# Kernel tuning notes

Hardware: AMD Instinct MI355X
Metric: run time of the kernel (lower is better)

The kernel has to match this reference:

```python
import jax, jax.numpy as jnp
import numpy as np

WS = 8            # window_size
SHIFT = WS // 2   # cyclic shift for 'SW' type
HEAD_DIM = 32

def _rel_index(ws):
    # pairwise relative coordinate indices within a window, offset to [0, 2ws-2]
    cord = np.array([[i, j] for i in range(ws) for j in range(ws)])
    rel = cord[:, None, :] - cord[None, :, :] + ws - 1
    return rel[:, :, 0], rel[:, :, 1]

def _shift_mask(h_w, w_w, p):
    # boolean attention mask for shifted windows; True = masked (-inf)
    s = p - SHIFT
    m = np.zeros((h_w, w_w, p, p, p, p), dtype=bool)
    m[-1, :, :s, :, s:, :] = True
    m[-1, :, s:, :, :s, :] = True
    m[:, -1, :, :s, :, s:] = True
    m[:, -1, :, s:, :, :s] = True
    return m.reshape(h_w * w_w, p * p, p * p)

def setup_inputs() -> dict:
    key = jax.random.key(0)
    ks = jax.random.split(key, 6)
    b, H, W, c = 4, 256, 256, 256
    nh = c // HEAD_DIM
    return {
        "x": jax.random.normal(ks[0], (b, H, W, c), jnp.float32),
        "W_qkv": jax.random.normal(ks[1], (c, 3 * c), jnp.float32) * 0.02,
        "b_qkv": jnp.zeros((3 * c,), jnp.float32),
        "rel_pos": jax.random.normal(ks[2], (nh, 2 * WS - 1, 2 * WS - 1), jnp.float32) * 0.02,
        "W_out": jax.random.normal(ks[3], (c, c), jnp.float32) * 0.02,
        "b_out": jnp.zeros((c,), jnp.float32),
    }

def reference(x, W_qkv, b_qkv, rel_pos, W_out, b_out):
    b, H, W, c = x.shape
    nh = c // HEAD_DIM
    scale = HEAD_DIM ** -0.5
    # cyclic shift (type == 'SW')
    x = jnp.roll(x, (-SHIFT, -SHIFT), axis=(1, 2))
    hw, ww = H // WS, W // WS
    nw, p2 = hw * ww, WS * WS
    # partition into windows: [b, nw, p2, c]
    xw = x.reshape(b, hw, WS, ww, WS, c).transpose(0, 1, 3, 2, 4, 5).reshape(b, nw, p2, c)
    # QKV projection; layout of out dim is (3, n_heads, head_dim)
    qkv = (xw @ W_qkv + b_qkv).reshape(b, nw, p2, 3, nh, HEAD_DIM)
    q, k, v = qkv[..., 0, :, :], qkv[..., 1, :, :], qkv[..., 2, :, :]
    # attention scores per head/window: [h, b, nw, p2, p2]
    sim = jnp.einsum('bwphc,bwqhc->hbwpq', q, k) * scale
    ri, rj = _rel_index(WS)
    sim = sim + rel_pos[:, ri, rj][:, None, None]            # relative position bias
    mask = jnp.asarray(_shift_mask(hw, ww, WS))              # [nw, p2, p2]
    sim = jnp.where(mask[None, None], -jnp.inf, sim)
    probs = jax.nn.softmax(sim, axis=-1)
    out = jnp.einsum('hbwpq,bwqhc->bwphc', probs, v).reshape(b, nw, p2, nh * HEAD_DIM)
    out = out @ W_out + b_out
    # un-window: [b, H, W, c_out]
    out = out.reshape(b, hw, ww, WS, WS, -1).transpose(0, 1, 3, 2, 4, 5).reshape(b, H, W, -1)
    return jnp.roll(out, (SHIFT, SHIFT), axis=(1, 2))
```

## Files before the change

kernel.cpp:

```cpp
#include <hip/hip_runtime.h>
#include <hip/hip_bf16.h>

typedef __attribute__((ext_vector_type(4))) float f32x4;
typedef __attribute__((ext_vector_type(2))) unsigned int u32x2;
typedef __attribute__((ext_vector_type(8))) short s16x8;
typedef __attribute__((ext_vector_type(8))) __bf16 bf16v8;
typedef __attribute__((ext_vector_type(8))) _Float16 f16v8;
typedef __attribute__((ext_vector_type(4))) _Float16 f16x4;

#define LDS_XS 0
#define LDS_QS 32768
#define LDS_KS 65536
#define LDS_VT 98304
#define LDS_TOT 131072

__device__ __forceinline__ f32x4 mfma16(s16x8 a, s16x8 b, f32x4 c) {
  return __builtin_amdgcn_mfma_f32_16x16x32_bf16(
      __builtin_bit_cast(bf16v8, a), __builtin_bit_cast(bf16v8, b), c, 0, 0, 0);
}
__device__ __forceinline__ f32x4 mfma16h(s16x8 a, s16x8 b, f32x4 c) {
  return __builtin_amdgcn_mfma_f32_16x16x32_f16(
      __builtin_bit_cast(f16v8, a), __builtin_bit_cast(f16v8, b), c, 0, 0, 0);
}
__device__ __forceinline__ f32x4 mfmah16(f16x4 a, f16x4 b, f32x4 c) {
  return __builtin_amdgcn_mfma_f32_16x16x16f16(a, b, c, 0, 0, 0);
}

__device__ __forceinline__ unsigned int cvt2(float a, float b) {
  __hip_bfloat162 r = __float22bfloat162_rn(make_float2(a, b));
  unsigned int u;
  __builtin_memcpy(&u, &r, 4);
  return u;
}
__device__ __forceinline__ unsigned int cvt2h(float a, float b) {
  auto r = __builtin_amdgcn_cvt_pkrtz(a, b);
  unsigned int u;
  __builtin_memcpy(&u, &r, 4);
  return u;
}
__device__ __forceinline__ f16x4 pack4h(float a, float b, float c, float d) {
  u32x2 u;
  u.x = cvt2h(a, b);
  u.y = cvt2h(c, d);
  f16x4 r;
  __builtin_memcpy(&r, &u, 8);
  return r;
}

__device__ __forceinline__ short f2bf(float f) {
  unsigned u = __float_as_uint(f);
  u += 0x7fffu + ((u >> 16) & 1u);
  return (short)(u >> 16);
}

__device__ __forceinline__ int swz512(int row, int colByte) {
  return row * 512 + (colByte ^ ((row & 7) << 4));
}
__device__ __forceinline__ int swz128(int row, int colByte) {
  return row * 128 + (colByte ^ ((row & 7) << 4));
}

__global__ void prep_w(const float* __restrict__ Wqkv, const float* __restrict__ Wout,
                       const float* __restrict__ relp,
                       short* __restrict__ wqkvT, short* __restrict__ wH,
                       float* __restrict__ relt) {
  int t = blockIdx.x * 256 + threadIdx.x;
  if (t < 768 * 256) {
    int n = t >> 8, k = t & 255;
    wqkvT[t] = f2bf(Wqkv[k * 768 + n]);
  } else if (t < 768 * 256 + 256 * 256) {
    int t2 = t - 768 * 256;
    int n = t2 >> 8, k = t2 & 255;
    _Float16 h = (_Float16)Wout[k * 256 + n];
    unsigned short us;
    __builtin_memcpy(&us, &h, 2);
    wH[t2] = (short)us;
  } else {
    int u = t - 768 * 256 - 256 * 256;
    int r = u & 3, l = (u >> 2) & 63, strip = (u >> 8) & 3;
    int qt = (u >> 10) & 3, h = (u >> 12) & 7, var = (u >> 15) & 3;
    int p = strip * 16 + (l & 15);
    int q = qt * 16 + ((l >> 4) << 2) + r;
    int pi = p >> 3, pj = p & 7, qi = q >> 3, qj = q & 7;
    bool mrow = (var >> 1) & 1, mcol = var & 1;
    bool mk = (mrow && ((pi < 4) != (qi < 4))) || (mcol && ((pj < 4) != (qj < 4)));
    relt[u] = mk ? -1e30f : relp[h * 225 + (pi - qi + 7) * 15 + (pj - qj + 7)];
  }
}

__global__ __launch_bounds__(512, 2) void swin_mfma(
    const float* __restrict__ x, const float* __restrict__ bqkv,
    const float* __restrict__ bout,
    const short* __restrict__ wqkvT, const short* __restrict__ wH,
    const float* __restrict__ relt, float* __restrict__ out)
{
  __shared__ __align__(16) char lds[LDS_TOT];

  const int tx = threadIdx.x;
  const int w  = tx >> 6;
  const int l  = tx & 63;
  const int g  = l >> 4;
  const int li = l & 15;

  const int b   = blockIdx.x >> 10;
  const int wdw = blockIdx.x & 1023;
  const int wh  = wdw >> 5, wwi = wdw & 31;
  const int rvar = ((wh == 31) ? 2 : 0) | ((wwi == 31) ? 1 : 0);
  const int phalf = w & 1, p0 = phalf * 32;

  for (int i = 0; i < 8; ++i) {
    int idx = tx + i * 512;
    int p = idx >> 6, c4 = idx & 63;
    int pi = p >> 3, pj = p & 7;
    int sr = (wh * 8 + pi + 4) & 255;
    int sc = (wwi * 8 + pj + 4) & 255;
    f32x4 v = *(const f32x4*)(x + ((((size_t)b * 256 + sr) * 256 + sc) * 256 + c4 * 4));
    u32x2 uu;
    uu.x = cvt2(v[0], v[1]);
    uu.y = cvt2(v[2], v[3]);
    *(u32x2*)(lds + LDS_XS + swz512(p, c4 * 8)) = uu;
  }

  int ocol[6];
  #pragma unroll
  for (int j = 0; j < 4; ++j) ocol[j] = (w * 4 + j) * 16 + li;
  #pragma unroll
  for (int j = 4; j < 6; ++j) ocol[j] = 512 + (w * 2 + (j - 4)) * 16 + li;
  s16x8 bcur[6];
  #pragma unroll
  for (int j = 0; j < 6; ++j)
    bcur[j] = *(const s16x8*)(wqkvT + (size_t)ocol[j] * 256 + g * 8);

  __syncthreads();

  {
    f32x4 acc[6][4];
    #pragma unroll
    for (int j = 0; j < 6; ++j)
      #pragma unroll
      for (int rb = 0; rb < 4; ++rb)
        acc[j][rb] = (f32x4){0.f, 0.f, 0.f, 0.f};

    s16x8 a[2][4];
    #pragma unroll
    for (int rb = 0; rb < 4; ++rb)
      a[0][rb] = *(const s16x8*)(lds + LDS_XS + swz512(rb * 16 + li, g * 16));

    #pragma unroll
    for (int kk = 0; kk < 8; ++kk) {
      const int cur = kk & 1;
      s16x8 bnext[6];
      if (kk < 7) {
        #pragma unroll
        for (int rb = 0; rb < 4; ++rb)
          a[cur ^ 1][rb] = *(const s16x8*)(lds + LDS_XS
                                           + swz512(rb * 16 + li, (kk + 1) * 64 + g * 16));
        #pragma unroll
        for (int j = 0; j < 6; ++j)
          bnext[j] = *(const s16x8*)(wqkvT + (size_t)ocol[j] * 256 + (kk + 1) * 32 + g * 8);
      }
      #pragma unroll
      for (int j = 0; j < 4; ++j)
        #pragma unroll
        for (int rb = 0; rb < 4; ++rb)
          acc[j][rb] = mfma16(bcur[j], a[cur][rb], acc[j][rb]);
      #pragma unroll
      for (int j = 4; j < 6; ++j)
        #pragma unroll
        for (int rb = 0; rb < 4; ++rb)
          acc[j][rb] = mfma16(a[cur][rb], bcur[j], acc[j][rb]);
      if (kk < 7) {
        #pragma unroll
        for (int j = 0; j < 6; ++j) bcur[j] = bnext[j];
      }
    }

    #pragma unroll
    for (int j = 0; j < 4; ++j) {
      const int cb = w * 4 + j;
      if (cb < 16) {
        f32x4 bq = *(const f32x4*)(bqkv + cb * 16 + g * 4);
        #pragma unroll
        for (int rb = 0; rb < 4; ++rb) {
          const float SC = 0.17677669529663687f;
          u32x2 uu;
          uu.x = cvt2((acc[j][rb][0] + bq[0]) * SC, (acc[j][rb][1] + bq[1]) * SC);
          uu.y = cvt2((acc[j][rb][2] + bq[2]) * SC, (acc[j][rb][3] + bq[3]) * SC);
          *(u32x2*)(lds + LDS_QS + swz512(rb * 16 + li, cb * 32 + g * 8)) = uu;
        }
      } else {
        f32x4 bk = *(const f32x4*)(bqkv + cb * 16 + g * 4);
        #pragma unroll
        for (int rb = 0; rb < 4; ++rb) {
          u32x2 uu;
          uu.x = cvt2(acc[j][rb][0] + bk[0], acc[j][rb][1] + bk[1]);
          uu.y = cvt2(acc[j][rb][2] + bk[2], acc[j][rb][3] + bk[3]);
          *(u32x2*)(lds + LDS_KS + swz512(rb * 16 + li, (cb - 16) * 32 + g * 8)) = uu;
        }
      }
    }
    #pragma unroll
    for (int j = 4; j < 6; ++j) {
      const int d = (w * 2 + (j - 4)) * 16 + li;
      const float bv = bqkv[512 + d];
      #pragma unroll
      for (int rb = 0; rb < 4; ++rb) {
        u32x2 uu;
        uu.x = cvt2h(acc[j][rb][0] + bv, acc[j][rb][1] + bv);
        uu.y = cvt2h(acc[j][rb][2] + bv, acc[j][rb][3] + bv);
        *(u32x2*)(lds + LDS_VT + swz128(d, rb * 32 + g * 8)) = uu;
      }
    }
  }

  f32x4 rc2[2][2][4];
  #pragma unroll
  for (int u = 0; u < 2; ++u) {
    const int h = (w >> 1) + u * 4;
    #pragma unroll
    for (int pt = 0; pt < 2; ++pt)
      #pragma unroll
      for (int qt = 0; qt < 4; ++qt)
        rc2[u][pt][qt] = *(const f32x4*)(relt
            + ((((rvar * 8 + h) * 4 + qt) * 4 + (phalf * 2 + pt)) * 64 + l) * 4);
  }

  __syncthreads();

  {
    s16x8 qf2[2][2], kf2[2][4];
    f16x4 vf2[2][2][4];
    #pragma unroll
    for (int u = 0; u < 2; ++u) {
      const int h = (w >> 1) + u * 4;
      #pragma unroll
      for (int pt = 0; pt < 2; ++pt)
        qf2[u][pt] = *(const s16x8*)(lds + LDS_QS + swz512(p0 + pt * 16 + li, h * 64 + g * 16));
      #pragma unroll
      for (int qt = 0; qt < 4; ++qt)
        kf2[u][qt] = *(const s16x8*)(lds + LDS_KS + swz512(qt * 16 + li, h * 64 + g * 16));
      #pragma unroll
      for (int dt = 0; dt < 2; ++dt)
        #pragma unroll
        for (int qt = 0; qt < 4; ++qt)
          vf2[u][dt][qt] = *(const f16x4*)(lds + LDS_VT
                                           + swz128(h * 32 + dt * 16 + li, qt * 32 + g * 8));
    }

    #pragma unroll
    for (int u = 0; u < 2; ++u) {
      const int h = (w >> 1) + u * 4;

      f32x4 simT[2][4];
      #pragma unroll
      for (int pt = 0; pt < 2; ++pt)
        #pragma unroll
        for (int qt = 0; qt < 4; ++qt)
          simT[pt][qt] = mfma16(kf2[u][qt], qf2[u][pt], rc2[u][pt][qt]);

      float rinv[2];
      f16x4 pa[2][4];
      #pragma unroll
      for (int pt = 0; pt < 2; ++pt) {
        float s = 0.f;
        #pragma unroll
        for (int qt = 0; qt < 4; ++qt) {
          float e0 = __expf(simT[pt][qt][0]);
          float e1 = __expf(simT[pt][qt][1]);
          float e2 = __expf(simT[pt][qt][2]);
          float e3 = __expf(simT[pt][qt][3]);
          s += (e0 + e1) + (e2 + e3);
          pa[pt][qt] = pack4h(e0, e1, e2, e3);
        }
        s += __shfl_xor(s, 16);
        s += __shfl_xor(s, 32);
        rinv[pt] = 1.0f / s;
      }

      f32x4 at[2][2];
      #pragma unroll
      for (int pt = 0; pt < 2; ++pt)
        #pragma unroll
        for (int dt = 0; dt < 2; ++dt)
          at[pt][dt] = (f32x4){0.f, 0.f, 0.f, 0.f};
      #pragma unroll
      for (int qt = 0; qt < 4; ++qt)
        #pragma unroll
        for (int pt = 0; pt < 2; ++pt)
          #pragma unroll
          for (int dt = 0; dt < 2; ++dt)
            at[pt][dt] = mfmah16(vf2[u][dt][qt], pa[pt][qt], at[pt][dt]);

      #pragma unroll
      for (int pt = 0; pt < 2; ++pt)
        #pragma unroll
        for (int dt = 0; dt < 2; ++dt) {
          const f32x4 a4 = at[pt][dt];
          u32x2 hh;
          hh.x = cvt2h(a4[0] * rinv[pt], a4[1] * rinv[pt]);
          hh.y = cvt2h(a4[2] * rinv[pt], a4[3] * rinv[pt]);
          *(u32x2*)(lds + LDS_XS + swz512(p0 + pt * 16 + li, h * 64 + dt * 32 + g * 8)) = hh;
        }
    }
  }

  s16x8 bc[2];
  #pragma unroll
  for (int c = 0; c < 2; ++c)
    bc[c] = *(const s16x8*)(wH + (size_t)((w * 2 + c) * 16 + li) * 256 + g * 8);

  __syncthreads();

  {
    f32x4 acc2[2][4];
    #pragma unroll
    for (int c = 0; c < 2; ++c)
      #pragma unroll
      for (int rb = 0; rb < 4; ++rb)
        acc2[c][rb] = (f32x4){0.f, 0.f, 0.f, 0.f};

    s16x8 a[2][4];
    #pragma unroll
    for (int rb = 0; rb < 4; ++rb)
      a[0][rb] = *(const s16x8*)(lds + LDS_XS + swz512(rb * 16 + li, g * 16));

    #pragma unroll
    for (int kk = 0; kk < 8; ++kk) {
      const int cur = kk & 1;
      s16x8 bn[2];
      if (kk < 7) {
        #pragma unroll
        for (int rb = 0; rb < 4; ++rb)
          a[cur ^ 1][rb] = *(const s16x8*)(lds + LDS_XS
                                           + swz512(rb * 16 + li, (kk + 1) * 64 + g * 16));
        #pragma unroll
        for (int c = 0; c < 2; ++c)
          bn[c] = *(const s16x8*)(wH + (size_t)((w * 2 + c) * 16 + li) * 256
                                  + (kk + 1) * 32 + g * 8);
      }
      #pragma unroll
      for (int c = 0; c < 2; ++c)
        #pragma unroll
        for (int rb = 0; rb < 4; ++rb)
          acc2[c][rb] = mfma16h(a[cur][rb], bc[c], acc2[c][rb]);
      if (kk < 7) {
        #pragma unroll
        for (int c = 0; c < 2; ++c) bc[c] = bn[c];
      }
    }

    #pragma unroll
    for (int c = 0; c < 2; ++c) {
      const int n = (w * 2 + c) * 16 + li;
      const float bo = bout[n];
      #pragma unroll
      for (int rb = 0; rb < 4; ++rb)
        #pragma unroll
        for (int r = 0; r < 4; ++r) {
          int m = rb * 16 + g * 4 + r;
          int pi = m >> 3, pj = m & 7;
          int dr = (wh * 8 + pi + 4) & 255;
          int dc = (wwi * 8 + pj + 4) & 255;
          out[(((size_t)b * 256 + dr) * 256 + dc) * 256 + n] = acc2[c][rb][r] + bo;
        }
    }
  }
}

extern "C" void kernel_launch(void* const* d_in, const int* in_sizes, int n_in,
                              void* d_out, int out_size, void* d_ws, size_t ws_size,
                              hipStream_t stream) {
  (void)in_sizes; (void)n_in; (void)out_size; (void)ws_size;
  const float* x    = (const float*)d_in[0];
  const float* Wqkv = (const float*)d_in[1];
  const float* bqkv = (const float*)d_in[2];
  const float* relp = (const float*)d_in[3];
  const float* Wout = (const float*)d_in[4];
  const float* bout = (const float*)d_in[5];
  float* out = (float*)d_out;

  short* wqkvT = (short*)d_ws;
  short* wH    = wqkvT + 768 * 256;
  float* relt  = (float*)(wH + 256 * 256);

  hipLaunchKernelGGL(prep_w, dim3(1536), dim3(256), 0, stream,
                     Wqkv, Wout, relp, wqkvT, wH, relt);
  hipLaunchKernelGGL(swin_mfma, dim3(4096), dim3(512), 0, stream,
                     x, bqkv, bout, wqkvT, wH, relt, out);
}
```

Baseline: 397.7 us.

## Make swin kernel persistent over 16 windows with async prefetch of next window

The kernel now launches 256 blocks that each loop over 16 consecutive windows instead of one block per window. During the output projection of each window, the next window's fp32 input is fetched straight into LDS with global_load_lds, then converted to bf16 after a barrier. The aim is to hide global input latency behind MFMA work and to avoid per-block launch and prologue costs. The trade-off is that 256 blocks at 2 blocks/CU may underfill the GPU, and the loop adds extra barriers and a serial convert step per window.

```diff
diff --git a/kernel.cpp b/kernel.cpp
--- a/kernel.cpp
+++ b/kernel.cpp
@@ -88,6 +88,38 @@
   }
 }
 
+__device__ __forceinline__ void stage_x_async(const float* __restrict__ x, int win,
+                                              int w, int l, char* lds) {
+  const int b = win >> 10, wdw = win & 1023;
+  const int wh = wdw >> 5, wwi = wdw & 31;
+  #pragma unroll
+  for (int i = 0; i < 8; ++i) {
+    const int chunk = (w * 8 + i) * 64 + l;
+    const int p = chunk >> 6, c4 = chunk & 63;
+    const int pi = p >> 3, pj = p & 7;
+    const int sr = (wh * 8 + pi + 4) & 255;
+    const int sc = (wwi * 8 + pj + 4) & 255;
+    const float* gsrc = x + ((((size_t)b * 256 + sr) * 256 + sc) * 256 + c4 * 4);
+    __builtin_amdgcn_global_load_lds(
+        (const __attribute__((address_space(1))) void*)gsrc,
+        (__attribute__((address_space(3))) void*)(lds + LDS_QS + (w * 8 + i) * 1024),
+        16, 0, 0);
+  }
+}
+
+__device__ __forceinline__ void convert_x(int tx, char* lds) {
+  #pragma unroll
+  for (int i = 0; i < 8; ++i) {
+    const int chunk = tx + i * 512;
+    f32x4 v = *(const f32x4*)(lds + LDS_QS + chunk * 16);
+    const int p = chunk >> 6, c4 = chunk & 63;
+    u32x2 uu;
+    uu.x = cvt2(v[0], v[1]);
+    uu.y = cvt2(v[2], v[3]);
+    *(u32x2*)(lds + LDS_XS + swz512(p, c4 * 8)) = uu;
+  }
+}
+
 __global__ __launch_bounds__(512, 2) void swin_mfma(
     const float* __restrict__ x, const float* __restrict__ bqkv,
     const float* __restrict__ bout,
@@ -101,268 +133,271 @@
   const int l  = tx & 63;
   const int g  = l >> 4;
   const int li = l & 15;
-
-  const int b   = blockIdx.x >> 10;
-  const int wdw = blockIdx.x & 1023;
-  const int wh  = wdw >> 5, wwi = wdw & 31;
-  const int rvar = ((wh == 31) ? 2 : 0) | ((wwi == 31) ? 1 : 0);
   const int phalf = w & 1, p0 = phalf * 32;
-
-  for (int i = 0; i < 8; ++i) {
-    int idx = tx + i * 512;
-    int p = idx >> 6, c4 = idx & 63;
-    int pi = p >> 3, pj = p & 7;
-    int sr = (wh * 8 + pi + 4) & 255;
-    int sc = (wwi * 8 + pj + 4) & 255;
-    f32x4 v = *(const f32x4*)(x + ((((size_t)b * 256 + sr) * 256 + sc) * 256 + c4 * 4));
-    u32x2 uu;
-    uu.x = cvt2(v[0], v[1]);
-    uu.y = cvt2(v[2], v[3]);
-    *(u32x2*)(lds + LDS_XS + swz512(p, c4 * 8)) = uu;
-  }
 
   int ocol[6];
   #pragma unroll
   for (int j = 0; j < 4; ++j) ocol[j] = (w * 4 + j) * 16 + li;
   #pragma unroll
   for (int j = 4; j < 6; ++j) ocol[j] = 512 + (w * 2 + (j - 4)) * 16 + li;
-  s16x8 bcur[6];
-  #pragma unroll
-  for (int j = 0; j < 6; ++j)
-    bcur[j] = *(const s16x8*)(wqkvT + (size_t)ocol[j] * 256 + g * 8);
-
+
+  stage_x_async(x, blockIdx.x * 16, w, l, lds);
   __syncthreads();
-
-  {
-    f32x4 acc[6][4];
-    #pragma unroll
-    for (int j = 0; j < 6; ++j)
+  convert_x(tx, lds);
+  __syncthreads();
+
+  #pragma unroll 1
+  for (int wi = 0; wi < 16; ++wi) {
+    const int win = blockIdx.x * 16 + wi;
+    const int b   = win >> 10;
+    const int wdw = win & 1023;
+    const int wh  = wdw >> 5, wwi = wdw & 31;
+    const int rvar = ((wh == 31) ? 2 : 0) | ((wwi == 31) ? 1 : 0);
+
+    {
+      f32x4 acc[6][4];
+      #pragma unroll
+      for (int j = 0; j < 6; ++j)
+        #pragma unroll
+        for (int rb = 0; rb < 4; ++rb)
+          acc[j][rb] = (f32x4){0.f, 0.f, 0.f, 0.f};
+
+      s16x8 bcur[6];
+      #pragma unroll
+      for (int j = 0; j < 6; ++j)
+        bcur[j] = *(const s16x8*)(wqkvT + (size_t)ocol[j] * 256 + g * 8);
+
+      s16x8 a[2][4];
       #pragma unroll
       for (int rb = 0; rb < 4; ++rb)
-        acc[j][rb] = (f32x4){0.f, 0.f, 0.f, 0.f};
-
-    s16x8 a[2][4];
-    #pragma unroll
-    for (int rb = 0; rb < 4; ++rb)
-      a[0][rb] = *(const s16x8*)(lds + LDS_XS + swz512(rb * 16 + li, g * 16));
-
-    #pragma unroll
-    for (int kk = 0; kk < 8; ++kk) {
-      const int cur = kk & 1;
-      s16x8 bnext[6];
-      if (kk < 7) {
-        #pragma unroll
-        for (int rb = 0; rb < 4; ++rb)
-          a[cur ^ 1][rb] = *(const s16x8*)(lds + LDS_XS
-                                           + swz512(rb * 16 + li, (kk + 1) * 64 + g * 16));
-        #pragma unroll
-        for (int j = 0; j < 6; ++j)
-          bnext[j] = *(const s16x8*)(wqkvT + (size_t)ocol[j] * 256 + (kk + 1) * 32 + g * 8);
-      }
-      #pragma unroll
-      for (int j = 0; j < 4; ++j)
-        #pragma unroll
-        for (int rb = 0; rb < 4; ++rb)
-          acc[j][rb] = mfma16(bcur[j], a[cur][rb], acc[j][rb]);
-      #pragma unroll
-      for (int j = 4; j < 6; ++j)
-        #pragma unroll
-        for (int rb = 0; rb < 4; ++rb)
-          acc[j][rb] = mfma16(a[cur][rb], bcur[j], acc[j][rb]);
-      if (kk < 7) {
-        #pragma unroll
-        for (int j = 0; j < 6; ++j) bcur[j] = bnext[j];
-      }
-    }
-
-    #pragma unroll
-    for (int j = 0; j < 4; ++j) {
-      const int cb = w * 4 + j;
-      if (cb < 16) {
-        f32x4 bq = *(const f32x4*)(bqkv + cb * 16 + g * 4);
-        #pragma unroll
-        for (int rb = 0; rb < 4; ++rb) {
-          const float SC = 0.17677669529663687f;
-          u32x2 uu;
-          uu.x = cvt2((acc[j][rb][0] + bq[0]) * SC, (acc[j][rb][1] + bq[1]) * SC);
-          uu.y = cvt2((acc[j][rb][2] + bq[2]) * SC, (acc[j][rb][3] + bq[3]) * SC);
-          *(u32x2*)(lds + LDS_QS + swz512(rb * 16 + li, cb * 32 + g * 8)) = uu;
-        }
-      } else {
-        f32x4 bk = *(const f32x4*)(bqkv + cb * 16 + g * 4);
+        a[0][rb] = *(const s16x8*)(lds + LDS_XS + swz512(rb * 16 + li, g * 16));
+
+      #pragma unroll
+      for (int kk = 0; kk < 8; ++kk) {
+        const int cur = kk & 1;
+        s16x8 bnext[6];
+        if (kk < 7) {
+          #pragma unroll
+          for (int rb = 0; rb < 4; ++rb)
+            a[cur ^ 1][rb] = *(const s16x8*)(lds + LDS_XS
+                                             + swz512(rb * 16 + li, (kk + 1) * 64 + g * 16));
+          #pragma unroll
+          for (int j = 0; j < 6; ++j)
+            bnext[j] = *(const s16x8*)(wqkvT + (size_t)ocol[j] * 256 + (kk + 1) * 32 + g * 8);
+        }
+        #pragma unroll
+        for (int j = 0; j < 4; ++j)
+          #pragma unroll
+          for (int rb = 0; rb < 4; ++rb)
+            acc[j][rb] = mfma16(bcur[j], a[cur][rb], acc[j][rb]);
+        #pragma unroll
+        for (int j = 4; j < 6; ++j)
+          #pragma unroll
+          for (int rb = 0; rb < 4; ++rb)
+            acc[j][rb] = mfma16(a[cur][rb], bcur[j], acc[j][rb]);
+        if (kk < 7) {
+          #pragma unroll
+          for (int j = 0; j < 6; ++j) bcur[j] = bnext[j];
+        }
+      }
+
+      #pragma unroll
+      for (int j = 0; j < 4; ++j) {
+        const int cb = w * 4 + j;
+        if (cb < 16) {
+          f32x4 bq = *(const f32x4*)(bqkv + cb * 16 + g * 4);
+          #pragma unroll
+          for (int rb = 0; rb < 4; ++rb) {
+            const float SC = 0.17677669529663687f;
+            u32x2 uu;
+            uu.x = cvt2((acc[j][rb][0] + bq[0]) * SC, (acc[j][rb][1] + bq[1]) * SC);
+            uu.y = cvt2((acc[j][rb][2] + bq[2]) * SC, (acc[j][rb][3] + bq[3]) * SC);
+            *(u32x2*)(lds + LDS_QS + swz512(rb * 16 + li, cb * 32 + g * 8)) = uu;
+          }
+        } else {
+          f32x4 bk = *(const f32x4*)(bqkv + cb * 16 + g * 4);
+          #pragma unroll
+          for (int rb = 0; rb < 4; ++rb) {
+            u32x2 uu;
+            uu.x = cvt2(acc[j][rb][0] + bk[0], acc[j][rb][1] + bk[1]);
+            uu.y = cvt2(acc[j][rb][2] + bk[2], acc[j][rb][3] + bk[3]);
+            *(u32x2*)(lds + LDS_KS + swz512(rb * 16 + li, (cb - 16) * 32 + g * 8)) = uu;
+          }
+        }
+      }
+      #pragma unroll
+      for (int j = 4; j < 6; ++j) {
+        const int d = (w * 2 + (j - 4)) * 16 + li;
+        const float bv = bqkv[512 + d];
         #pragma unroll
         for (int rb = 0; rb < 4; ++rb) {
           u32x2 uu;
-          uu.x = cvt2(acc[j][rb][0] + bk[0], acc[j][rb][1] + bk[1]);
-          uu.y = cvt2(acc[j][rb][2] + bk[2], acc[j][rb][3] + bk[3]);
-          *(u32x2*)(lds + LDS_KS + swz512(rb * 16 + li, (cb - 16) * 32 + g * 8)) = uu;
+          uu.x = cvt2h(acc[j][rb][0] + bv, acc[j][rb][1] + bv);
+          uu.y = cvt2h(acc[j][rb][2] + bv, acc[j][rb][3] + bv);
+          *(u32x2*)(lds + LDS_VT + swz128(d, rb * 32 + g * 8)) = uu;
         }
       }
     }
-    #pragma unroll
-    for (int j = 4; j < 6; ++j) {
-      const int d = (w * 2 + (j - 4)) * 16 + li;
-      const float bv = bqkv[512 + d];
-      #pragma unroll
-      for (int rb = 0; rb < 4; ++rb) {
-        u32x2 uu;
-        uu.x = cvt2h(acc[j][rb][0] + bv, acc[j][rb][1] + bv);
-        uu.y = cvt2h(acc[j][rb][2] + bv, acc[j][rb][3] + bv);
-        *(u32x2*)(lds + LDS_VT + swz128(d, rb * 32 + g * 8)) = uu;
-      }
-    }
-  }
-
-  f32x4 rc2[2][2][4];
-  #pragma unroll
-  for (int u = 0; u < 2; ++u) {
-    const int h = (w >> 1) + u * 4;
-    #pragma unroll
-    for (int pt = 0; pt < 2; ++pt)
-      #pragma unroll
-      for (int qt = 0; qt < 4; ++qt)
-        rc2[u][pt][qt] = *(const f32x4*)(relt
-            + ((((rvar * 8 + h) * 4 + qt) * 4 + (phalf * 2 + pt)) * 64 + l) * 4);
-  }
-
-  __syncthreads();
-
-  {
-    s16x8 qf2[2][2], kf2[2][4];
-    f16x4 vf2[2][2][4];
+
+    f32x4 rc2[2][2][4];
     #pragma unroll
     for (int u = 0; u < 2; ++u) {
       const int h = (w >> 1) + u * 4;
       #pragma unroll
       for (int pt = 0; pt < 2; ++pt)
-        qf2[u][pt] = *(const s16x8*)(lds + LDS_QS + swz512(p0 + pt * 16 + li, h * 64 + g * 16));
-      #pragma unroll
-      for (int qt = 0; qt < 4; ++qt)
-        kf2[u][qt] = *(const s16x8*)(lds + LDS_KS + swz512(qt * 16 + li, h * 64 + g * 16));
-      #pragma unroll
-      for (int dt = 0; dt < 2; ++dt)
         #pragma unroll
         for (int qt = 0; qt < 4; ++qt)
-          vf2[u][dt][qt] = *(const f16x4*)(lds + LDS_VT
-                                           + swz128(h * 32 + dt * 16 + li, qt * 32 + g * 8));
+          rc2[u][pt][qt] = *(const f32x4*)(relt
+              + ((((rvar * 8 + h) * 4 + qt) * 4 + (phalf * 2 + pt)) * 64 + l) * 4);
     }
 
-    #pragma unroll
-    for (int u = 0; u < 2; ++u) {
-      const int h = (w >> 1) + u * 4;
-
-      f32x4 simT[2][4];
-      #pragma unroll
-      for (int pt = 0; pt < 2; ++pt)
+    __syncthreads();
+
+    {
+      s16x8 qf2[2][2], kf2[2][4];
+      f16x4 vf2[2][2][4];
+      #pragma unroll
+      for (int u = 0; u < 2; ++u) {
+        const int h = (w >> 1) + u * 4;
+        #pragma unroll
+        for (int pt = 0; pt < 2; ++pt)
+          qf2[u][pt] = *(const s16x8*)(lds + LDS_QS + swz512(p0 + pt * 16 + li, h * 64 + g * 16));
         #pragma unroll
         for (int qt = 0; qt < 4; ++qt)
-          simT[pt][qt] = mfma16(kf2[u][qt], qf2[u][pt], rc2[u][pt][qt]);
-
-      float rinv[2];
-      f16x4 pa[2][4];
-      #pragma unroll
-      for (int pt = 0; pt < 2; ++pt) {
-        float s = 0.f;
-        #pragma unroll
-        for (int qt = 0; qt < 4; ++qt) {
-          float e0 = __expf(simT[pt][qt][0]);
-          float e1 = __expf(simT[pt][qt][1]);
-          float e2 = __expf(simT[pt][qt][2]);
-          float e3 = __expf(simT[pt][qt][3]);
-          s += (e0 + e1) + (e2 + e3);
-          pa[pt][qt] = pack4h(e0, e1, e2, e3);
-        }
-        s += __shfl_xor(s, 16);
-        s += __shfl_xor(s, 32);
-        rinv[pt] = 1.0f / s;
-      }
-
-      f32x4 at[2][2];
-      #pragma unroll
-      for (int pt = 0; pt < 2; ++pt)
+          kf2[u][qt] = *(const s16x8*)(lds + LDS_KS + swz512(qt * 16 + li, h * 64 + g * 16));
         #pragma unroll
         for (int dt = 0; dt < 2; ++dt)
-          at[pt][dt] = (f32x4){0.f, 0.f, 0.f, 0.f};
-      #pragma unroll
-      for (int qt = 0; qt < 4; ++qt)
+          #pragma unroll
+          for (int qt = 0; qt < 4; ++qt)
+            vf2[u][dt][qt] = *(const f16x4*)(lds + LDS_VT
+                                             + swz128(h * 32 + dt * 16 + li, qt * 32 + g * 8));
+      }
+
+      #pragma unroll
+      for (int u = 0; u < 2; ++u) {
+        const int h = (w >> 1) + u * 4;
+
+        f32x4 simT[2][4];
         #pragma unroll
         for (int pt = 0; pt < 2; ++pt)
           #pragma unroll
+          for (int qt = 0; qt < 4; ++qt)
+            simT[pt][qt] = mfma16(kf2[u][qt], qf2[u][pt], rc2[u][pt][qt]);
+
+        float rinv[2];
+        f16x4 pa[2][4];
+        #pragma unroll
+        for (int pt = 0; pt < 2; ++pt) {
+          float s = 0.f;
+          #pragma unroll
+          for (int qt = 0; qt < 4; ++qt) {
+            float e0 = __expf(simT[pt][qt][0]);
+            float e1 = __expf(simT[pt][qt][1]);
+            float e2 = __expf(simT[pt][qt][2]);
+            float e3 = __expf(simT[pt][qt][3]);
+            s += (e0 + e1) + (e2 + e3);
+            pa[pt][qt] = pack4h(e0, e1, e2, e3);
+          }
+          s += __shfl_xor(s, 16);
+          s += __shfl_xor(s, 32);
+          rinv[pt] = 1.0f / s;
+        }
+
+        f32x4 at[2][2];
+        #pragma unroll
+        for (int pt = 0; pt < 2; ++pt)
+          #pragma unroll
           for (int dt = 0; dt < 2; ++dt)
-            at[pt][dt] = mfmah16(vf2[u][dt][qt], pa[pt][qt], at[pt][dt]);
-
-      #pragma unroll
-      for (int pt = 0; pt < 2; ++pt)
-        #pragma unroll
-        for (int dt = 0; dt < 2; ++dt) {
-          const f32x4 a4 = at[pt][dt];
-          u32x2 hh;
-          hh.x = cvt2h(a4[0] * rinv[pt], a4[1] * rinv[pt]);
-          hh.y = cvt2h(a4[2] * rinv[pt], a4[3] * rinv[pt]);
-          *(u32x2*)(lds + LDS_XS + swz512(p0 + pt * 16 + li, h * 64 + dt * 32 + g * 8)) = hh;
-        }
+            at[pt][dt] = (f32x4){0.f, 0.f, 0.f, 0.f};
+        #pragma unroll
+        for (int qt = 0; qt < 4; ++qt)
+          #pragma unroll
+          for (int pt = 0; pt < 2; ++pt)
+            #pragma unroll
+            for (int dt = 0; dt < 2; ++dt)
+              at[pt][dt] = mfmah16(vf2[u][dt][qt], pa[pt][qt], at[pt][dt]);
+
+        #pragma unroll
+        for (int pt = 0; pt < 2; ++pt)
+          #pragma unroll
+          for (int dt = 0; dt < 2; ++dt) {
+            const f32x4 a4 = at[pt][dt];
+            u32x2 hh;
+            hh.x = cvt2h(a4[0] * rinv[pt], a4[1] * rinv[pt]);
+            hh.y = cvt2h(a4[2] * rinv[pt], a4[3] * rinv[pt]);
+            *(u32x2*)(lds + LDS_XS + swz512(p0 + pt * 16 + li, h * 64 + dt * 32 + g * 8)) = hh;
+          }
+      }
     }
-  }
-
-  s16x8 bc[2];
-  #pragma unroll
-  for (int c = 0; c < 2; ++c)
-    bc[c] = *(const s16x8*)(wH + (size_t)((w * 2 + c) * 16 + li) * 256 + g * 8);
-
-  __syncthreads();
-
-  {
-    f32x4 acc2[2][4];
+
+    s16x8 bc[2];
     #pragma unroll
     for (int c = 0; c < 2; ++c)
+      bc[c] = *(const s16x8*)(wH + (size_t)((w * 2 + c) * 16 + li) * 256 + g * 8);
+
+    __syncthreads();
+
+    {
+      if (wi < 15) stage_x_async(x, win + 1, w, l, lds);
+
+      f32x4 acc2[2][4];
+      #pragma unroll
+      for (int c = 0; c < 2; ++c)
+        #pragma unroll
+        for (int rb = 0; rb < 4; ++rb)
+          acc2[c][rb] = (f32x4){0.f, 0.f, 0.f, 0.f};
+
+      s16x8 a[2][4];
       #pragma unroll
       for (int rb = 0; rb < 4; ++rb)
-        acc2[c][rb] = (f32x4){0.f, 0.f, 0.f, 0.f};
-
-    s16x8 a[2][4];
-    #pragma unroll
-    for (int rb = 0; rb < 4; ++rb)
-      a[0][rb] = *(const s16x8*)(lds + LDS_XS + swz512(rb * 16 + li, g * 16));
-
-    #pragma unroll
-    for (int kk = 0; kk < 8; ++kk) {
-      const int cur = kk & 1;
-      s16x8 bn[2];
-      if (kk < 7) {
+        a[0][rb] = *(const s16x8*)(lds + LDS_XS + swz512(rb * 16 + li, g * 16));
+
+      #pragma unroll
+      for (int kk = 0; kk < 8; ++kk) {
+        const int cur = kk & 1;
+        s16x8 bn[2];
+        if (kk < 7) {
+          #pragma unroll
+          for (int rb = 0; rb < 4; ++rb)
+            a[cur ^ 1][rb] = *(const s16x8*)(lds + LDS_XS
+                                             + swz512(rb * 16 + li, (kk + 1) * 64 + g * 16));
+          #pragma unroll
+          for (int c = 0; c < 2; ++c)
+            bn[c] = *(const s16x8*)(wH + (size_t)((w * 2 + c) * 16 + li) * 256
+                                    + (kk + 1) * 32 + g * 8);
+        }
+        #pragma unroll
+        for (int c = 0; c < 2; ++c)
+          #pragma unroll
+          for (int rb = 0; rb < 4; ++rb)
+            acc2[c][rb] = mfma16h(a[cur][rb], bc[c], acc2[c][rb]);
+        if (kk < 7) {
+          #pragma unroll
+          for (int c = 0; c < 2; ++c) bc[c] = bn[c];
+        }
+      }
+
+      #pragma unroll
+      for (int c = 0; c < 2; ++c) {
+        const int n = (w * 2 + c) * 16 + li;
+        const float bo = bout[n];
         #pragma unroll
         for (int rb = 0; rb < 4; ++rb)
-          a[cur ^ 1][rb] = *(const s16x8*)(lds + LDS_XS
-                                           + swz512(rb * 16 + li, (kk + 1) * 64 + g * 16));
-        #pragma unroll
-        for (int c = 0; c < 2; ++c)
-          bn[c] = *(const s16x8*)(wH + (size_t)((w * 2 + c) * 16 + li) * 256
-                                  + (kk + 1) * 32 + g * 8);
-      }
-      #pragma unroll
-      for (int c = 0; c < 2; ++c)
-        #pragma unroll
-        for (int rb = 0; rb < 4; ++rb)
-          acc2[c][rb] = mfma16h(a[cur][rb], bc[c], acc2[c][rb]);
-      if (kk < 7) {
-        #pragma unroll
-        for (int c = 0; c < 2; ++c) bc[c] = bn[c];
+          #pragma unroll
+          for (int r = 0; r < 4; ++r) {
+            int m = rb * 16 + g * 4 + r;
+            int pi = m >> 3, pj = m & 7;
+            int dr = (wh * 8 + pi + 4) & 255;
+            int dc = (wwi * 8 + pj + 4) & 255;
+            out[(((size_t)b * 256 + dr) * 256 + dc) * 256 + n] = acc2[c][rb][r] + bo;
+          }
       }
     }
-
-    #pragma unroll
-    for (int c = 0; c < 2; ++c) {
-      const int n = (w * 2 + c) * 16 + li;
-      const float bo = bout[n];
-      #pragma unroll
-      for (int rb = 0; rb < 4; ++rb)
-        #pragma unroll
-        for (int r = 0; r < 4; ++r) {
-          int m = rb * 16 + g * 4 + r;
-          int pi = m >> 3, pj = m & 7;
-          int dr = (wh * 8 + pi + 4) & 255;
-          int dc = (wwi * 8 + pj + 4) & 255;
-          out[(((size_t)b * 256 + dr) * 256 + dc) * 256 + n] = acc2[c][rb][r] + bo;
-        }
+    __syncthreads();
+
+    if (wi < 15) {
+      convert_x(tx, lds);
+      __syncthreads();
     }
   }
 }
@@ -385,6 +420,6 @@
 
   hipLaunchKernelGGL(prep_w, dim3(1536), dim3(256), 0, stream,
                      Wqkv, Wout, relp, wqkvT, wH, relt);
-  hipLaunchKernelGGL(swin_mfma, dim3(4096), dim3(512), 0, stream,
+  hipLaunchKernelGGL(swin_mfma, dim3(256), dim3(512), 0, stream,
                      x, bqkv, bout, wqkvT, wH, relt, out);
 }
```

Result: slower. 563.4 us (+41.7%).
